# Optimization experiments

Measured on AMD Instinct MI355X. Metric: run time of the kernel, lower is better.

Reference implementation:

```python
import jax, jax.numpy as jnp
import numpy as np

KERNEL = 128
STRIDE = 64


def setup_inputs() -> dict:
    key = jax.random.key(0)
    k1, k2, k3 = jax.random.split(key, 3)
    in_features = 8192
    fold_num = (in_features - KERNEL) // STRIDE + 1  # 127
    local_features = 128
    batch = 2048
    x = jax.random.normal(k1, (batch, in_features), dtype=jnp.float32)
    # stacked per-window Linear weights/biases (PyTorch Linear: y = x @ W.T + b)
    bound = 1.0 / np.sqrt(KERNEL)
    W = jax.random.uniform(k2, (fold_num, local_features, KERNEL), dtype=jnp.float32,
                           minval=-bound, maxval=bound)
    b = jax.random.uniform(k3, (fold_num, local_features), dtype=jnp.float32,
                           minval=-bound, maxval=bound)
    return {"x": x, "W": W, "b": b}


def reference(x, W, b):
    fold_num = W.shape[0]
    # window gather indices: [fold_num, kernel]
    idx = STRIDE * jnp.arange(fold_num)[:, None] + jnp.arange(KERNEL)[None, :]
    windows = x[:, idx]                      # [batch, fold_num, kernel]
    # per-window linear: out[b,f,l] = sum_k windows[b,f,k] * W[f,l,k] + b[f,l]
    out = jnp.einsum('bfk,flk->bfl', windows, W) + b[None, :, :]
    # concat along feature dim as in torch.cat(..., 1)
    return out.reshape(out.shape[0], -1)     # [batch, fold_num*local_features]
```

## Files before the change

kernel.cpp:

```cpp
#include <hip/hip_runtime.h>
#include <hip/hip_bf16.h>

typedef float f32x4 __attribute__((ext_vector_type(4)));
typedef __bf16 bf16x8 __attribute__((ext_vector_type(8)));

#define INF   8192
#define FOLDS 127
#define LOCAL 128
#define OUTF  (FOLDS * LOCAL)
#define BM    128

__global__ __launch_bounds__(256, 2)
void local_linear_kernel(const float* __restrict__ x,
                         const float* __restrict__ W,
                         const float* __restrict__ bias,
                         float* __restrict__ out)
{
    __shared__ __align__(16) __bf16 As[128 * 128];
    __shared__ __align__(16) __bf16 Bs[128 * 128];

    const int mt = blockIdx.x;
    const int f  = blockIdx.y;
    const int t  = threadIdx.x;

    const int m0 = mt * BM;
    const float* __restrict__ xg = x + (size_t)m0 * INF + (size_t)f * 64;
    const float* __restrict__ Wf = W + (size_t)f * (LOCAL * 128);

    #pragma unroll
    for (int it = 0; it < 8; ++it) {
        const int e   = it * 2048 + t * 8;
        const int row = e >> 7;
        const int col = e & 127;
        const float* g = xg + (size_t)row * INF + col;
        f32x4 v0 = *(const f32x4*)g;
        f32x4 v1 = *(const f32x4*)(g + 4);
        bf16x8 w;
        w[0] = (__bf16)v0[0]; w[1] = (__bf16)v0[1];
        w[2] = (__bf16)v0[2]; w[3] = (__bf16)v0[3];
        w[4] = (__bf16)v1[0]; w[5] = (__bf16)v1[1];
        w[6] = (__bf16)v1[2]; w[7] = (__bf16)v1[3];
        const int byte = (row * 256 + col * 2) ^ ((row & 7) << 4);
        *(bf16x8*)((char*)As + byte) = w;
    }
    #pragma unroll
    for (int it = 0; it < 8; ++it) {
        const int e   = it * 2048 + t * 8;
        const int row = e >> 7;
        const int col = e & 127;
        const float* g = Wf + row * 128 + col;
        f32x4 v0 = *(const f32x4*)g;
        f32x4 v1 = *(const f32x4*)(g + 4);
        bf16x8 w;
        w[0] = (__bf16)v0[0]; w[1] = (__bf16)v0[1];
        w[2] = (__bf16)v0[2]; w[3] = (__bf16)v0[3];
        w[4] = (__bf16)v1[0]; w[5] = (__bf16)v1[1];
        w[6] = (__bf16)v1[2]; w[7] = (__bf16)v1[3];
        const int byte = (row * 256 + col * 2) ^ ((row & 7) << 4);
        *(bf16x8*)((char*)Bs + byte) = w;
    }
    __syncthreads();

    const int lane = t & 63;
    const int wid  = t >> 6;
    const int wm   = wid >> 1;
    const int wn   = wid & 1;
    const int r16  = lane & 15;
    const int kq   = lane >> 4;

    f32x4 acc[4][4];
    #pragma unroll
    for (int i = 0; i < 4; ++i)
        #pragma unroll
        for (int j = 0; j < 4; ++j)
            acc[i][j] = (f32x4){0.f, 0.f, 0.f, 0.f};

    #pragma unroll
    for (int ks = 0; ks < 4; ++ks) {
        const int kof = ks * 32 + kq * 8;
        bf16x8 a[4], b[4];
        #pragma unroll
        for (int i = 0; i < 4; ++i) {
            const int row  = wm * 64 + i * 16 + r16;
            const int byte = (row * 256 + kof * 2) ^ ((row & 7) << 4);
            a[i] = *(const bf16x8*)((const char*)As + byte);
        }
        #pragma unroll
        for (int j = 0; j < 4; ++j) {
            const int row  = wn * 64 + j * 16 + r16;
            const int byte = (row * 256 + kof * 2) ^ ((row & 7) << 4);
            b[j] = *(const bf16x8*)((const char*)Bs + byte);
        }
        #pragma unroll
        for (int i = 0; i < 4; ++i)
            #pragma unroll
            for (int j = 0; j < 4; ++j)
                acc[i][j] = __builtin_amdgcn_mfma_f32_16x16x32_bf16(a[i], b[j], acc[i][j], 0, 0, 0);
    }

    float bv[4];
    #pragma unroll
    for (int j = 0; j < 4; ++j)
        bv[j] = bias[f * LOCAL + wn * 64 + j * 16 + r16];

    #pragma unroll
    for (int i = 0; i < 4; ++i) {
        const int mrow = m0 + wm * 64 + i * 16 + kq * 4;
        #pragma unroll
        for (int j = 0; j < 4; ++j) {
            const int ncol = f * LOCAL + wn * 64 + j * 16 + r16;
            float* o = out + (size_t)mrow * OUTF + ncol;
            #pragma unroll
            for (int r = 0; r < 4; ++r)
                o[(size_t)r * OUTF] = acc[i][j][r] + bv[j];
        }
    }
}

extern "C" void kernel_launch(void* const* d_in, const int* in_sizes, int n_in,
                              void* d_out, int out_size, void* d_ws, size_t ws_size,
                              hipStream_t stream) {
    const float* x    = (const float*)d_in[0];
    const float* W    = (const float*)d_in[1];
    const float* bias = (const float*)d_in[2];
    float* out        = (float*)d_out;

    dim3 grid(2048 / BM, FOLDS);
    dim3 block(256);
    local_linear_kernel<<<grid, block, 0, stream>>>(x, W, bias, out);
}
```

Before: 47.53 us.

## Process two adjacent folds per block sharing overlapping x window, pre-convert W to bf16

Each block now handles two adjacent folds, loading a 192-column x strip once so the 64-column overlap between windows is fetched only once. A separate pre-pass converts W to bf16 in the workspace, and the main kernel stages it into LDS with direct global-to-LDS loads. This halves the grid and raises LDS use per block, which may lower occupancy. The fold-1 compute also waits behind an extra sync and weight restage.

```diff
diff --git a/kernel.cpp b/kernel.cpp
--- a/kernel.cpp
+++ b/kernel.cpp
@@ -10,56 +10,44 @@
 #define OUTF  (FOLDS * LOCAL)
 #define BM    128
 
+#define WB_BYTES ((size_t)FOLDS * LOCAL * 128 * 2)
+
+__global__ void convert_w_kernel(const float* __restrict__ W, __bf16* __restrict__ Wb) {
+    const size_t i = ((size_t)blockIdx.x * 256 + threadIdx.x) * 8;
+    f32x4 v0 = *(const f32x4*)(W + i);
+    f32x4 v1 = *(const f32x4*)(W + i + 4);
+    bf16x8 w;
+    w[0] = (__bf16)v0[0]; w[1] = (__bf16)v0[1]; w[2] = (__bf16)v0[2]; w[3] = (__bf16)v0[3];
+    w[4] = (__bf16)v1[0]; w[5] = (__bf16)v1[1]; w[6] = (__bf16)v1[2]; w[7] = (__bf16)v1[3];
+    *(bf16x8*)(Wb + i) = w;
+}
+
+__device__ __forceinline__ void cvt_store8(char* lds, int byte, f32x4 v0, f32x4 v1) {
+    bf16x8 w;
+    w[0] = (__bf16)v0[0]; w[1] = (__bf16)v0[1]; w[2] = (__bf16)v0[2]; w[3] = (__bf16)v0[3];
+    w[4] = (__bf16)v1[0]; w[5] = (__bf16)v1[1]; w[6] = (__bf16)v1[2]; w[7] = (__bf16)v1[3];
+    *(bf16x8*)(lds + byte) = w;
+}
+
+template<bool WBF16>
 __global__ __launch_bounds__(256, 2)
 void local_linear_kernel(const float* __restrict__ x,
-                         const float* __restrict__ W,
+                         const float* __restrict__ Wf32,
+                         const __bf16* __restrict__ Wbf,
                          const float* __restrict__ bias,
                          float* __restrict__ out)
 {
-    __shared__ __align__(16) __bf16 As[128 * 128];
+    __shared__ __align__(16) __bf16 As[128 * 192];
     __shared__ __align__(16) __bf16 Bs[128 * 128];
 
     const int mt = blockIdx.x;
-    const int f  = blockIdx.y;
+    const int fg = blockIdx.y;
+    const int f0 = fg * 2;
+    const bool has_f1 = (f0 + 1) < FOLDS;
     const int t  = threadIdx.x;
 
     const int m0 = mt * BM;
-    const float* __restrict__ xg = x + (size_t)m0 * INF + (size_t)f * 64;
-    const float* __restrict__ Wf = W + (size_t)f * (LOCAL * 128);
-
-    #pragma unroll
-    for (int it = 0; it < 8; ++it) {
-        const int e   = it * 2048 + t * 8;
-        const int row = e >> 7;
-        const int col = e & 127;
-        const float* g = xg + (size_t)row * INF + col;
-        f32x4 v0 = *(const f32x4*)g;
-        f32x4 v1 = *(const f32x4*)(g + 4);
-        bf16x8 w;
-        w[0] = (__bf16)v0[0]; w[1] = (__bf16)v0[1];
-        w[2] = (__bf16)v0[2]; w[3] = (__bf16)v0[3];
-        w[4] = (__bf16)v1[0]; w[5] = (__bf16)v1[1];
-        w[6] = (__bf16)v1[2]; w[7] = (__bf16)v1[3];
-        const int byte = (row * 256 + col * 2) ^ ((row & 7) << 4);
-        *(bf16x8*)((char*)As + byte) = w;
-    }
-    #pragma unroll
-    for (int it = 0; it < 8; ++it) {
-        const int e   = it * 2048 + t * 8;
-        const int row = e >> 7;
-        const int col = e & 127;
-        const float* g = Wf + row * 128 + col;
-        f32x4 v0 = *(const f32x4*)g;
-        f32x4 v1 = *(const f32x4*)(g + 4);
-        bf16x8 w;
-        w[0] = (__bf16)v0[0]; w[1] = (__bf16)v0[1];
-        w[2] = (__bf16)v0[2]; w[3] = (__bf16)v0[3];
-        w[4] = (__bf16)v1[0]; w[5] = (__bf16)v1[1];
-        w[6] = (__bf16)v1[2]; w[7] = (__bf16)v1[3];
-        const int byte = (row * 256 + col * 2) ^ ((row & 7) << 4);
-        *(bf16x8*)((char*)Bs + byte) = w;
-    }
-    __syncthreads();
+    const float* __restrict__ xg = x + (size_t)m0 * INF + (size_t)f0 * 64;
 
     const int lane = t & 63;
     const int wid  = t >> 6;
@@ -68,52 +56,116 @@
     const int r16  = lane & 15;
     const int kq   = lane >> 4;
 
-    f32x4 acc[4][4];
-    #pragma unroll
-    for (int i = 0; i < 4; ++i)
-        #pragma unroll
-        for (int j = 0; j < 4; ++j)
-            acc[i][j] = (f32x4){0.f, 0.f, 0.f, 0.f};
+    auto stageB = [&](int f) {
+        if constexpr (WBF16) {
+            const char* Wsrc = (const char*)(Wbf + (size_t)f * LOCAL * 128);
+            #pragma unroll
+            for (int c = 0; c < 8; ++c) {
+                const int base  = wid * 8192 + c * 1024;
+                const int b     = base + lane * 16;
+                const int row   = b >> 8;
+                const int inner = b & 255;
+                const int srcb  = row * 256 + (inner ^ ((row & 7) << 4));
+                __builtin_amdgcn_global_load_lds(
+                    (const __attribute__((address_space(1))) void*)(Wsrc + srcb),
+                    (__attribute__((address_space(3))) void*)((char*)Bs + base),
+                    16, 0, 0);
+            }
+        } else {
+            const float* Wf = Wf32 + (size_t)f * LOCAL * 128;
+            #pragma unroll
+            for (int it = 0; it < 8; ++it) {
+                const int e = it * 2048 + t * 8;
+                const int row = e >> 7, col = e & 127;
+                const float* g = Wf + row * 128 + col;
+                f32x4 v0 = *(const f32x4*)g;
+                f32x4 v1 = *(const f32x4*)(g + 4);
+                cvt_store8((char*)Bs, (row * 256 + col * 2) ^ ((row & 7) << 4), v0, v1);
+            }
+        }
+    };
+
+    stageB(f0);
 
     #pragma unroll
-    for (int ks = 0; ks < 4; ++ks) {
-        const int kof = ks * 32 + kq * 8;
-        bf16x8 a[4], b[4];
+    for (int it = 0; it < 8; ++it) {
+        const int e = it * 2048 + t * 8;
+        const int row = e >> 7, col = e & 127;
+        const float* g = xg + (size_t)row * INF + col;
+        f32x4 v0 = *(const f32x4*)g;
+        f32x4 v1 = *(const f32x4*)(g + 4);
+        cvt_store8((char*)As, (row * 384 + col * 2) ^ ((row & 7) << 4), v0, v1);
+    }
+    if (has_f1) {
         #pragma unroll
-        for (int i = 0; i < 4; ++i) {
-            const int row  = wm * 64 + i * 16 + r16;
-            const int byte = (row * 256 + kof * 2) ^ ((row & 7) << 4);
-            a[i] = *(const bf16x8*)((const char*)As + byte);
+        for (int it = 0; it < 4; ++it) {
+            const int e = it * 2048 + t * 8;
+            const int row = e >> 6, col = 128 + (e & 63);
+            const float* g = xg + (size_t)row * INF + col;
+            f32x4 v0 = *(const f32x4*)g;
+            f32x4 v1 = *(const f32x4*)(g + 4);
+            cvt_store8((char*)As, (row * 384 + col * 2) ^ ((row & 7) << 4), v0, v1);
         }
-        #pragma unroll
-        for (int j = 0; j < 4; ++j) {
-            const int row  = wn * 64 + j * 16 + r16;
-            const int byte = (row * 256 + kof * 2) ^ ((row & 7) << 4);
-            b[j] = *(const bf16x8*)((const char*)Bs + byte);
-        }
+    }
+
+    auto computeFold = [&](int f, int acolBase) {
+        f32x4 acc[4][4];
         #pragma unroll
         for (int i = 0; i < 4; ++i)
             #pragma unroll
             for (int j = 0; j < 4; ++j)
-                acc[i][j] = __builtin_amdgcn_mfma_f32_16x16x32_bf16(a[i], b[j], acc[i][j], 0, 0, 0);
-    }
+                acc[i][j] = (f32x4){0.f, 0.f, 0.f, 0.f};
 
-    float bv[4];
-    #pragma unroll
-    for (int j = 0; j < 4; ++j)
-        bv[j] = bias[f * LOCAL + wn * 64 + j * 16 + r16];
+        #pragma unroll
+        for (int ks = 0; ks < 4; ++ks) {
+            const int kof = ks * 32 + kq * 8;
+            bf16x8 a[4], b[4];
+            #pragma unroll
+            for (int i = 0; i < 4; ++i) {
+                const int row  = wm * 64 + i * 16 + r16;
+                const int byte = (row * 384 + (acolBase + kof) * 2) ^ ((row & 7) << 4);
+                a[i] = *(const bf16x8*)((const char*)As + byte);
+            }
+            #pragma unroll
+            for (int j = 0; j < 4; ++j) {
+                const int row  = wn * 64 + j * 16 + r16;
+                const int byte = (row * 256 + kof * 2) ^ ((row & 7) << 4);
+                b[j] = *(const bf16x8*)((const char*)Bs + byte);
+            }
+            #pragma unroll
+            for (int i = 0; i < 4; ++i)
+                #pragma unroll
+                for (int j = 0; j < 4; ++j)
+                    acc[i][j] = __builtin_amdgcn_mfma_f32_16x16x32_bf16(a[i], b[j], acc[i][j], 0, 0, 0);
+        }
 
-    #pragma unroll
-    for (int i = 0; i < 4; ++i) {
-        const int mrow = m0 + wm * 64 + i * 16 + kq * 4;
+        float bv[4];
         #pragma unroll
-        for (int j = 0; j < 4; ++j) {
-            const int ncol = f * LOCAL + wn * 64 + j * 16 + r16;
-            float* o = out + (size_t)mrow * OUTF + ncol;
+        for (int j = 0; j < 4; ++j)
+            bv[j] = bias[f * LOCAL + wn * 64 + j * 16 + r16];
+
+        #pragma unroll
+        for (int i = 0; i < 4; ++i) {
+            const int mrow = m0 + wm * 64 + i * 16 + kq * 4;
             #pragma unroll
-            for (int r = 0; r < 4; ++r)
-                o[(size_t)r * OUTF] = acc[i][j][r] + bv[j];
+            for (int j = 0; j < 4; ++j) {
+                const int ncol = f * LOCAL + wn * 64 + j * 16 + r16;
+                float* o = out + (size_t)mrow * OUTF + ncol;
+                #pragma unroll
+                for (int r = 0; r < 4; ++r)
+                    o[(size_t)r * OUTF] = acc[i][j][r] + bv[j];
+            }
         }
+    };
+
+    __syncthreads();
+    computeFold(f0, 0);
+
+    if (has_f1) {
+        __syncthreads();
+        stageB(f0 + 1);
+        __syncthreads();
+        computeFold(f0 + 1, 64);
     }
 }
 
@@ -125,7 +177,14 @@
     const float* bias = (const float*)d_in[2];
     float* out        = (float*)d_out;
 
-    dim3 grid(2048 / BM, FOLDS);
+    dim3 grid(2048 / BM, 64);
     dim3 block(256);
-    local_linear_kernel<<<grid, block, 0, stream>>>(x, W, bias, out);
+
+    if (ws_size >= WB_BYTES) {
+        __bf16* Wb = (__bf16*)d_ws;
+        convert_w_kernel<<<1016, 256, 0, stream>>>(W, Wb);
+        local_linear_kernel<true><<<grid, block, 0, stream>>>(x, W, Wb, bias, out);
+    } else {
+        local_linear_kernel<false><<<grid, block, 0, stream>>>(x, W, nullptr, bias, out);
+    }
 }
```

Measured after the change: 50.06 us. +5.3%, slower.

## Reuse per-fold weight tile across four M tiles per block

Applied to the files above, without the earlier changes.

Each block now converts the fold's weight tile to bf16 in LDS once and loops over four 128-row tiles of x, cutting redundant W loads and conversions by a factor of four. The grid is reordered to put folds on the x dimension, and bias is folded into the accumulator initialisation. In exchange, the grid shrinks to 127x4 blocks, which may underfill the GPU. The x loads are also serialised behind syncthreads with no double buffering, so there is less overlap between memory and compute.

```diff
diff --git a/kernel.cpp b/kernel.cpp
--- a/kernel.cpp
+++ b/kernel.cpp
@@ -9,6 +9,14 @@
 #define LOCAL 128
 #define OUTF  (FOLDS * LOCAL)
 #define BM    128
+#define MT_PER_BLOCK 4
+
+__device__ __forceinline__ void cvt_store8(char* lds, int byte, f32x4 v0, f32x4 v1) {
+    bf16x8 w;
+    w[0] = (__bf16)v0[0]; w[1] = (__bf16)v0[1]; w[2] = (__bf16)v0[2]; w[3] = (__bf16)v0[3];
+    w[4] = (__bf16)v1[0]; w[5] = (__bf16)v1[1]; w[6] = (__bf16)v1[2]; w[7] = (__bf16)v1[3];
+    *(bf16x8*)(lds + byte) = w;
+}
 
 __global__ __launch_bounds__(256, 2)
 void local_linear_kernel(const float* __restrict__ x,
@@ -19,30 +27,18 @@
     __shared__ __align__(16) __bf16 As[128 * 128];
     __shared__ __align__(16) __bf16 Bs[128 * 128];
 
-    const int mt = blockIdx.x;
-    const int f  = blockIdx.y;
-    const int t  = threadIdx.x;
+    const int f = blockIdx.x;
+    const int c = blockIdx.y;
+    const int t = threadIdx.x;
 
-    const int m0 = mt * BM;
-    const float* __restrict__ xg = x + (size_t)m0 * INF + (size_t)f * 64;
+    const int lane = t & 63;
+    const int wid  = t >> 6;
+    const int wm   = wid >> 1;
+    const int wn   = wid & 1;
+    const int r16  = lane & 15;
+    const int kq   = lane >> 4;
+
     const float* __restrict__ Wf = W + (size_t)f * (LOCAL * 128);
-
-    #pragma unroll
-    for (int it = 0; it < 8; ++it) {
-        const int e   = it * 2048 + t * 8;
-        const int row = e >> 7;
-        const int col = e & 127;
-        const float* g = xg + (size_t)row * INF + col;
-        f32x4 v0 = *(const f32x4*)g;
-        f32x4 v1 = *(const f32x4*)(g + 4);
-        bf16x8 w;
-        w[0] = (__bf16)v0[0]; w[1] = (__bf16)v0[1];
-        w[2] = (__bf16)v0[2]; w[3] = (__bf16)v0[3];
-        w[4] = (__bf16)v1[0]; w[5] = (__bf16)v1[1];
-        w[6] = (__bf16)v1[2]; w[7] = (__bf16)v1[3];
-        const int byte = (row * 256 + col * 2) ^ ((row & 7) << 4);
-        *(bf16x8*)((char*)As + byte) = w;
-    }
     #pragma unroll
     for (int it = 0; it < 8; ++it) {
         const int e   = it * 2048 + t * 8;
@@ -51,51 +47,7 @@
         const float* g = Wf + row * 128 + col;
         f32x4 v0 = *(const f32x4*)g;
         f32x4 v1 = *(const f32x4*)(g + 4);
-        bf16x8 w;
-        w[0] = (__bf16)v0[0]; w[1] = (__bf16)v0[1];
-        w[2] = (__bf16)v0[2]; w[3] = (__bf16)v0[3];
-        w[4] = (__bf16)v1[0]; w[5] = (__bf16)v1[1];
-        w[6] = (__bf16)v1[2]; w[7] = (__bf16)v1[3];
-        const int byte = (row * 256 + col * 2) ^ ((row & 7) << 4);
-        *(bf16x8*)((char*)Bs + byte) = w;
-    }
-    __syncthreads();
-
-    const int lane = t & 63;
-    const int wid  = t >> 6;
-    const int wm   = wid >> 1;
-    const int wn   = wid & 1;
-    const int r16  = lane & 15;
-    const int kq   = lane >> 4;
-
-    f32x4 acc[4][4];
-    #pragma unroll
-    for (int i = 0; i < 4; ++i)
-        #pragma unroll
-        for (int j = 0; j < 4; ++j)
-            acc[i][j] = (f32x4){0.f, 0.f, 0.f, 0.f};
-
-    #pragma unroll
-    for (int ks = 0; ks < 4; ++ks) {
-        const int kof = ks * 32 + kq * 8;
-        bf16x8 a[4], b[4];
-        #pragma unroll
-        for (int i = 0; i < 4; ++i) {
-            const int row  = wm * 64 + i * 16 + r16;
-            const int byte = (row * 256 + kof * 2) ^ ((row & 7) << 4);
-            a[i] = *(const bf16x8*)((const char*)As + byte);
-        }
-        #pragma unroll
-        for (int j = 0; j < 4; ++j) {
-            const int row  = wn * 64 + j * 16 + r16;
-            const int byte = (row * 256 + kof * 2) ^ ((row & 7) << 4);
-            b[j] = *(const bf16x8*)((const char*)Bs + byte);
-        }
-        #pragma unroll
-        for (int i = 0; i < 4; ++i)
-            #pragma unroll
-            for (int j = 0; j < 4; ++j)
-                acc[i][j] = __builtin_amdgcn_mfma_f32_16x16x32_bf16(a[i], b[j], acc[i][j], 0, 0, 0);
+        cvt_store8((char*)Bs, (row * 256 + col * 2) ^ ((row & 7) << 4), v0, v1);
     }
 
     float bv[4];
@@ -103,17 +55,66 @@
     for (int j = 0; j < 4; ++j)
         bv[j] = bias[f * LOCAL + wn * 64 + j * 16 + r16];
 
-    #pragma unroll
-    for (int i = 0; i < 4; ++i) {
-        const int mrow = m0 + wm * 64 + i * 16 + kq * 4;
+    for (int im = 0; im < MT_PER_BLOCK; ++im) {
+        const int mt = c * MT_PER_BLOCK + im;
+        const int m0 = mt * BM;
+        const float* __restrict__ xg = x + (size_t)m0 * INF + (size_t)f * 64;
+
         #pragma unroll
-        for (int j = 0; j < 4; ++j) {
-            const int ncol = f * LOCAL + wn * 64 + j * 16 + r16;
-            float* o = out + (size_t)mrow * OUTF + ncol;
+        for (int it = 0; it < 8; ++it) {
+            const int e   = it * 2048 + t * 8;
+            const int row = e >> 7;
+            const int col = e & 127;
+            const float* g = xg + (size_t)row * INF + col;
+            f32x4 v0 = *(const f32x4*)g;
+            f32x4 v1 = *(const f32x4*)(g + 4);
+            cvt_store8((char*)As, (row * 256 + col * 2) ^ ((row & 7) << 4), v0, v1);
+        }
+        __syncthreads();
+
+        f32x4 acc[4][4];
+        #pragma unroll
+        for (int i = 0; i < 4; ++i)
             #pragma unroll
-            for (int r = 0; r < 4; ++r)
-                o[(size_t)r * OUTF] = acc[i][j][r] + bv[j];
+            for (int j = 0; j < 4; ++j)
+                acc[i][j] = (f32x4){bv[j], bv[j], bv[j], bv[j]};
+
+        #pragma unroll
+        for (int ks = 0; ks < 4; ++ks) {
+            const int kof = ks * 32 + kq * 8;
+            bf16x8 a[4], b[4];
+            #pragma unroll
+            for (int i = 0; i < 4; ++i) {
+                const int row  = wm * 64 + i * 16 + r16;
+                const int byte = (row * 256 + kof * 2) ^ ((row & 7) << 4);
+                a[i] = *(const bf16x8*)((const char*)As + byte);
+            }
+            #pragma unroll
+            for (int j = 0; j < 4; ++j) {
+                const int row  = wn * 64 + j * 16 + r16;
+                const int byte = (row * 256 + kof * 2) ^ ((row & 7) << 4);
+                b[j] = *(const bf16x8*)((const char*)Bs + byte);
+            }
+            #pragma unroll
+            for (int i = 0; i < 4; ++i)
+                #pragma unroll
+                for (int j = 0; j < 4; ++j)
+                    acc[i][j] = __builtin_amdgcn_mfma_f32_16x16x32_bf16(a[i], b[j], acc[i][j], 0, 0, 0);
         }
+
+        #pragma unroll
+        for (int i = 0; i < 4; ++i) {
+            const int mrow = m0 + wm * 64 + i * 16 + kq * 4;
+            #pragma unroll
+            for (int j = 0; j < 4; ++j) {
+                const int ncol = f * LOCAL + wn * 64 + j * 16 + r16;
+                float* o = out + (size_t)mrow * OUTF + ncol;
+                #pragma unroll
+                for (int r = 0; r < 4; ++r)
+                    o[(size_t)r * OUTF] = acc[i][j][r];
+            }
+        }
+        __syncthreads();
     }
 }
 
@@ -125,7 +126,7 @@
     const float* bias = (const float*)d_in[2];
     float* out        = (float*)d_out;
 
-    dim3 grid(2048 / BM, FOLDS);
+    dim3 grid(FOLDS, 2048 / (BM * MT_PER_BLOCK));
     dim3 block(256);
     local_linear_kernel<<<grid, block, 0, stream>>>(x, W, bias, out);
 }
```

New measurement: 55.08 us. 1.16x slower.
